# Performance work log

Hardware: AMD Instinct MI355X
Metric: run time of the kernel (lower is better)

Reference implementation:

```python
import jax, jax.numpy as jnp
import numpy as np

B, D, HID = 16384, 1024, 4096
HALF = D // 2


def setup_inputs() -> dict:
    key = jax.random.key(0)
    ks = jax.random.split(key, 9)
    sc_in = 1.0 / np.sqrt(HALF)
    sc_h = 1.0 / np.sqrt(HID)
    return {
        "z": jax.random.normal(ks[0], (B, D), dtype=jnp.float32),
        "W1s": jax.random.uniform(ks[1], (HALF, HID), jnp.float32, -sc_in, sc_in),
        "b1s": jax.random.uniform(ks[2], (HID,), jnp.float32, -sc_in, sc_in),
        "W2s": jax.random.uniform(ks[3], (HID, HALF), jnp.float32, -sc_h, sc_h),
        "b2s": jax.random.uniform(ks[4], (HALF,), jnp.float32, -sc_h, sc_h),
        "W1t": jax.random.uniform(ks[5], (HALF, HID), jnp.float32, -sc_in, sc_in),
        "b1t": jax.random.uniform(ks[6], (HID,), jnp.float32, -sc_in, sc_in),
        "W2t": jax.random.uniform(ks[7], (HID, HALF), jnp.float32, -sc_h, sc_h),
        "b2t": jax.random.uniform(ks[8], (HALF,), jnp.float32, -sc_h, sc_h),
    }


def reference(z, W1s, b1s, W2s, b2s, W1t, b1t, W2t, b2t):
    # mask_even=True: a = even-indexed features, b = odd-indexed features
    a = z[:, 0::2]  # [B, HALF]
    b = z[:, 1::2]  # [B, HALF]
    # two-layer MLPs for s and t (cond=None -> inp = a)
    s = jnp.maximum(a @ W1s + b1s, 0.0) @ W2s + b2s  # [B, HALF]
    t = jnp.maximum(a @ W1t + b1t, 0.0) @ W2t + b2t  # [B, HALF]
    b_out = b * jnp.exp(s) + t
    logdet = s.sum(axis=1)  # [B]
    # scatter back: a -> even slots, b_out -> odd slots (interleave)
    z_out = jnp.stack([a, b_out], axis=-1).reshape(z.shape)
    return z_out, logdet
```

## Files before the change

### kernel.cpp

```cpp
#include <hip/hip_runtime.h>
#include <hip/hip_bf16.h>
#include <cstdint>
#include <cstddef>

#define BROWS  16384
#define DDIM   1024
#define HID_N  4096
#define HALF_K 512
#define LDH    8192

typedef __attribute__((ext_vector_type(8))) short s8v;
typedef __attribute__((ext_vector_type(4))) float f4v;
typedef __attribute__((ext_vector_type(2))) float f2v;

__device__ __forceinline__ void gload16(const void* g, void* l) {
  __builtin_amdgcn_global_load_lds(
      (const __attribute__((address_space(1))) unsigned int*)g,
      (__attribute__((address_space(3))) unsigned int*)l, 16, 0, 0);
}
#define BAR()   asm volatile("s_barrier" ::: "memory")
#define BARS()  asm volatile("s_waitcnt lgkmcnt(0)\n\ts_barrier" ::: "memory")
#define SCHED0() __builtin_amdgcn_sched_barrier(0)

template <int N> __device__ __forceinline__ void vmw() {
  if constexpr (N == 0)      asm volatile("s_waitcnt vmcnt(0)" ::: "memory");
  else if constexpr (N == 4) asm volatile("s_waitcnt vmcnt(4)" ::: "memory");
  else if constexpr (N == 8) asm volatile("s_waitcnt vmcnt(8)" ::: "memory");
}

__device__ __forceinline__ void transpose_body(const float* __restrict__ W,
                                               __hip_bfloat16* __restrict__ WT,
                                               int K, int N, int bx, int by) {
  __shared__ float tile[32][33];
  const int n0 = bx * 32, k0 = by * 32;
  const int tx = threadIdx.x & 31;
  const int ty = threadIdx.x >> 5;
#pragma unroll
  for (int i = 0; i < 32; i += 8)
    tile[ty + i][tx] = W[(size_t)(k0 + ty + i) * N + n0 + tx];
  __syncthreads();
#pragma unroll
  for (int i = 0; i < 32; i += 8)
    WT[(size_t)(n0 + ty + i) * K + k0 + tx] = __float2bfloat16(tile[tx][ty + i]);
}

__global__ __launch_bounds__(256) void prep_kernel(const float* __restrict__ z,
                                                   __hip_bfloat16* __restrict__ a16,
                                                   const float* __restrict__ W1s,
                                                   const float* __restrict__ W1t,
                                                   const float* __restrict__ W2s,
                                                   const float* __restrict__ W2t,
                                                   __hip_bfloat16* __restrict__ w1T,
                                                   __hip_bfloat16* __restrict__ w2sT,
                                                   __hip_bfloat16* __restrict__ w2tT) {
  const int b = blockIdx.x;
  if (b < 4096) {
    const int idx = b * 256 + threadIdx.x;
    const int m  = idx >> 6;
    const int kb = idx & 63;
    const float4* zp = (const float4*)(z + (size_t)m * DDIM + (size_t)kb * 16);
    alignas(16) __hip_bfloat16 t[8];
#pragma unroll
    for (int i = 0; i < 4; ++i) {
      float4 v = zp[i];
      t[2 * i]     = __float2bfloat16(v.x);
      t[2 * i + 1] = __float2bfloat16(v.z);
    }
    *(s8v*)(a16 + (size_t)m * HALF_K + kb * 8) = *(const s8v*)t;
  } else if (b < 6144) {
    const int v = b - 4096;
    transpose_body(W1s, w1T, HALF_K, HID_N, v & 127, v >> 7);
  } else if (b < 8192) {
    const int v = b - 6144;
    transpose_body(W1t, w1T + (size_t)HID_N * HALF_K, HALF_K, HID_N, v & 127, v >> 7);
  } else if (b < 10240) {
    const int v = b - 8192;
    transpose_body(W2s, w2sT, HID_N, HALF_K, v & 15, v >> 4);
  } else {
    const int v = b - 10240;
    transpose_body(W2t, w2tT, HID_N, HALF_K, v & 15, v >> 4);
  }
}

__global__ __launch_bounds__(512, 2)
void gemm1_kernel(const __hip_bfloat16* __restrict__ A,
                  const __hip_bfloat16* __restrict__ BT,
                  const float* __restrict__ b1s, const float* __restrict__ b1t,
                  __hip_bfloat16* __restrict__ Hout) {
  __shared__ alignas(16) char smem[131072];
  constexpr int NT = HALF_K / 64;

  const int nwg = gridDim.x;
  const int orig = blockIdx.x;
  const int vid = (orig & 7) * (nwg >> 3) + (orig >> 3);
  const int bx = vid >> 5, by = vid & 31;
  const int m0 = bx * 256, n0 = by * 256;

  const int tid = threadIdx.x;
  const int trow = tid >> 3;
  const int scol = ((tid & 7) * 16) ^ ((trow & 7) << 4);

  const int lane = tid & 63, wid = tid >> 6;
  const int wr = wid >> 2, wc = wid & 3;
  const int lr = lane & 15, lk = lane >> 4;
  const int xo = (lr & 7) << 4;

  int aoff[4][2], boff[2][2];
#pragma unroll
  for (int j = 0; j < 4; ++j)
#pragma unroll
    for (int kk = 0; kk < 2; ++kk)
      aoff[j][kk] = (j * 32 + wr * 16 + lr) * 128 + ((kk * 64 + lk * 16) ^ xo);
#pragma unroll
  for (int nn = 0; nn < 2; ++nn)
#pragma unroll
    for (int kk = 0; kk < 2; ++kk)
      boff[nn][kk] = (nn * 64 + wc * 16 + lr) * 128 + ((kk * 64 + lk * 16) ^ xo);

  f4v acc[8][4] = {};

  auto stage_A = [&](int h, int T) {
#pragma unroll
    for (int l = 0; l < 2; ++l)
      gload16((const char*)A + (size_t)(m0 + h * 128 + l * 64 + trow) * (HALF_K * 2) + (size_t)T * 128 + scol,
              smem + (T & 1) * 65536 + h * 16384 + l * 8192 + tid * 16);
  };
  auto stage_B = [&](int h, int T) {
#pragma unroll
    for (int l = 0; l < 2; ++l)
      gload16((const char*)BT + (size_t)(n0 + h * 128 + l * 64 + trow) * (HALF_K * 2) + (size_t)T * 128 + scol,
              smem + (T & 1) * 65536 + 32768 + h * 16384 + l * 8192 + tid * 16);
  };

  stage_A(0, 0); stage_B(0, 0); stage_A(1, 0); stage_B(1, 0);
  stage_A(0, 1); stage_B(0, 1);
  vmw<4>();
  BAR();

  for (int T = 0; T < NT; ++T) {
    const char* bufp = smem + (T & 1) * 65536;
    s8v af[4][2], b0r[2][2], b1r[2][2];

#pragma unroll
    for (int j = 0; j < 4; ++j) {
      af[j][0] = *(const s8v*)(bufp + aoff[j][0]);
      af[j][1] = *(const s8v*)(bufp + aoff[j][1]);
    }
#pragma unroll
    for (int nn = 0; nn < 2; ++nn) {
      b0r[nn][0] = *(const s8v*)(bufp + 32768 + boff[nn][0]);
      b0r[nn][1] = *(const s8v*)(bufp + 32768 + boff[nn][1]);
    }
    if (T + 1 < NT) stage_B(1, T + 1);
    BAR(); SCHED0();
    __builtin_amdgcn_s_setprio(1);
#pragma unroll
    for (int j = 0; j < 4; ++j)
#pragma unroll
      for (int nn = 0; nn < 2; ++nn)
#pragma unroll
        for (int kk = 0; kk < 2; ++kk)
          acc[j][nn] = __builtin_amdgcn_mfma_f32_16x16x32_bf16(af[j][kk], b0r[nn][kk], acc[j][nn], 0, 0, 0);
    __builtin_amdgcn_s_setprio(0);
    BAR();

#pragma unroll
    for (int nn = 0; nn < 2; ++nn) {
      b1r[nn][0] = *(const s8v*)(bufp + 49152 + boff[nn][0]);
      b1r[nn][1] = *(const s8v*)(bufp + 49152 + boff[nn][1]);
    }
    if (T + 1 < NT) stage_A(1, T + 1);
    BAR(); SCHED0();
    __builtin_amdgcn_s_setprio(1);
#pragma unroll
    for (int j = 0; j < 4; ++j)
#pragma unroll
      for (int nn = 0; nn < 2; ++nn)
#pragma unroll
        for (int kk = 0; kk < 2; ++kk)
          acc[j][2 + nn] = __builtin_amdgcn_mfma_f32_16x16x32_bf16(af[j][kk], b1r[nn][kk], acc[j][2 + nn], 0, 0, 0);
    __builtin_amdgcn_s_setprio(0);
    BAR();

#pragma unroll
    for (int j = 0; j < 4; ++j) {
      af[j][0] = *(const s8v*)(bufp + 16384 + aoff[j][0]);
      af[j][1] = *(const s8v*)(bufp + 16384 + aoff[j][1]);
    }
    if (T + 2 < NT) stage_A(0, T + 2);
    BAR(); SCHED0();
    __builtin_amdgcn_s_setprio(1);
#pragma unroll
    for (int j = 0; j < 4; ++j)
#pragma unroll
      for (int nn = 0; nn < 2; ++nn)
#pragma unroll
        for (int kk = 0; kk < 2; ++kk)
          acc[4 + j][nn] = __builtin_amdgcn_mfma_f32_16x16x32_bf16(af[j][kk], b0r[nn][kk], acc[4 + j][nn], 0, 0, 0);
    __builtin_amdgcn_s_setprio(0);
    BAR();

    if (T + 2 < NT) stage_B(0, T + 2);
    SCHED0();
    __builtin_amdgcn_s_setprio(1);
#pragma unroll
    for (int j = 0; j < 4; ++j)
#pragma unroll
      for (int nn = 0; nn < 2; ++nn)
#pragma unroll
        for (int kk = 0; kk < 2; ++kk)
          acc[4 + j][2 + nn] = __builtin_amdgcn_mfma_f32_16x16x32_bf16(af[j][kk], b1r[nn][kk], acc[4 + j][2 + nn], 0, 0, 0);
    __builtin_amdgcn_s_setprio(0);
    if (T + 2 >= NT) vmw<0>(); else vmw<4>();
    BAR();
  }

  const float* bp = (n0 < HID_N) ? b1s : b1t;
  const int cb0 = n0 & (HID_N - 1);
  float bv[4];
#pragma unroll
  for (int ni = 0; ni < 4; ++ni) bv[ni] = bp[cb0 + ni * 64 + wc * 16 + lr];

#pragma unroll
  for (int mi = 0; mi < 8; ++mi) {
#pragma unroll
    for (int ni = 0; ni < 4; ++ni) {
      const int cb = (ni * 64 + wc * 16 + lr) * 2;
#pragma unroll
      for (int r = 0; r < 4; ++r) {
        const int row = mi * 32 + wr * 16 + lk * 4 + r;
        const int swz = ((row & 7) << 4) ^ (((row >> 3) & 1) << 8);
        float v = fmaxf(acc[mi][ni][r] + bv[ni], 0.0f);
        *(__hip_bfloat16*)(smem + row * 512 + (cb ^ swz)) = __float2bfloat16(v);
      }
    }
  }
  BARS();
#pragma unroll
  for (int i = 0; i < 16; ++i) {
    const int bo = tid * 16 + i * 8192;
    const int row = bo >> 9, cb = bo & 511;
    const int swz = ((row & 7) << 4) ^ (((row >> 3) & 1) << 8);
    s8v v = *(const s8v*)(smem + row * 512 + (cb ^ swz));
    *(s8v*)((char*)Hout + ((size_t)(m0 + row) * LDH + n0) * 2 + cb) = v;
  }
}

__global__ __launch_bounds__(512, 2)
void gemm2_kernel(const __hip_bfloat16* __restrict__ H,
                  const __hip_bfloat16* __restrict__ BsT,
                  const __hip_bfloat16* __restrict__ BtT,
                  const float* __restrict__ b2s, const float* __restrict__ b2t,
                  const float* __restrict__ zin, float* __restrict__ zout,
                  float* __restrict__ gpart) {
  __shared__ alignas(16) char smem[131072];
  constexpr int NT = HID_N / 64;

  const int nwg = gridDim.x;
  const int orig = blockIdx.x;
  const int vid = (orig & 7) * (nwg >> 3) + (orig >> 3);
  const int rb = vid >> 2, by = vid & 3;
  const int m0 = rb * 128, n0c = by * 128;

  const int tid = threadIdx.x;
  const int trow = tid >> 3;
  const int scol = ((tid & 7) * 16) ^ ((trow & 7) << 4);

  const int lane = tid & 63, wid = tid >> 6;
  const int ws = wid & 1, wc = (wid >> 1) & 1, wr = (wid >> 2) & 1;
  const int lr = lane & 15, lk = lane >> 4;
  const int xo = (lr & 7) << 4;

  const int aBase = ws ? 16384 : 0;
  const int bBase = ws ? 49152 : 32768;
  int aoff[4][2], boff[4][2];
#pragma unroll
  for (int f = 0; f < 4; ++f)
#pragma unroll
    for (int kk = 0; kk < 2; ++kk) {
      aoff[f][kk] = aBase + (wr * 64 + f * 16 + lr) * 128 + ((kk * 64 + lk * 16) ^ xo);
      boff[f][kk] = bBase + (wc * 64 + f * 16 + lr) * 128 + ((kk * 64 + lk * 16) ^ xo);
    }

  f4v acc[4][4] = {};

  auto stage_all = [&](int T) {
    char* dst = smem + (T & 1) * 65536;
    const size_t tcol = (size_t)T * 128 + scol;
#pragma unroll
    for (int l = 0; l < 2; ++l)
      gload16((const char*)H + (size_t)(m0 + l * 64 + trow) * (LDH * 2) + tcol,
              dst + l * 8192 + tid * 16);
#pragma unroll
    for (int l = 0; l < 2; ++l)
      gload16((const char*)H + (size_t)(m0 + l * 64 + trow) * (LDH * 2) + 8192 + tcol,
              dst + 16384 + l * 8192 + tid * 16);
#pragma unroll
    for (int l = 0; l < 2; ++l)
      gload16((const char*)BsT + (size_t)(n0c + l * 64 + trow) * (HID_N * 2) + tcol,
              dst + 32768 + l * 8192 + tid * 16);
#pragma unroll
    for (int l = 0; l < 2; ++l)
      gload16((const char*)BtT + (size_t)(n0c + l * 64 + trow) * (HID_N * 2) + tcol,
              dst + 49152 + l * 8192 + tid * 16);
  };

  stage_all(0);
  vmw<0>();
  BAR();

  for (int T = 0; T < NT; ++T) {
    const char* bufp = smem + (T & 1) * 65536;
    s8v af[4], bf[4];

#pragma unroll
    for (int f = 0; f < 4; ++f) af[f] = *(const s8v*)(bufp + aoff[f][0]);
#pragma unroll
    for (int f = 0; f < 4; ++f) bf[f] = *(const s8v*)(bufp + boff[f][0]);
    if (T + 1 < NT) stage_all(T + 1);
    __builtin_amdgcn_s_setprio(1);
#pragma unroll
    for (int fm = 0; fm < 4; ++fm)
#pragma unroll
      for (int fn = 0; fn < 4; ++fn)
        acc[fm][fn] = __builtin_amdgcn_mfma_f32_16x16x32_bf16(af[fm], bf[fn], acc[fm][fn], 0, 0, 0);
    __builtin_amdgcn_s_setprio(0);

#pragma unroll
    for (int f = 0; f < 4; ++f) af[f] = *(const s8v*)(bufp + aoff[f][1]);
#pragma unroll
    for (int f = 0; f < 4; ++f) bf[f] = *(const s8v*)(bufp + boff[f][1]);
    __builtin_amdgcn_s_setprio(1);
#pragma unroll
    for (int fm = 0; fm < 4; ++fm)
#pragma unroll
      for (int fn = 0; fn < 4; ++fn)
        acc[fm][fn] = __builtin_amdgcn_mfma_f32_16x16x32_bf16(af[fm], bf[fn], acc[fm][fn], 0, 0, 0);
    __builtin_amdgcn_s_setprio(0);

    if (T + 1 < NT) vmw<0>();
    BAR();
  }

  const float* bp2 = ws ? b2t : b2s;
  float bv[4];
#pragma unroll
  for (int fn = 0; fn < 4; ++fn) bv[fn] = bp2[n0c + wc * 64 + fn * 16 + lr];

  float* slds = (float*)smem;
  if (ws == 0) {
#pragma unroll
    for (int fm = 0; fm < 4; ++fm)
#pragma unroll
      for (int fn = 0; fn < 4; ++fn)
#pragma unroll
        for (int r = 0; r < 4; ++r) {
          const int row = wr * 64 + fm * 16 + lk * 4 + r;
          const int col = wc * 64 + fn * 16 + lr;
          slds[row * 128 + col] = acc[fm][fn][r] + bv[fn];
        }
  }
  BARS();
  if (ws == 1) {
    float pl[4][4] = {};
#pragma unroll
    for (int fm = 0; fm < 4; ++fm) {
#pragma unroll
      for (int fn = 0; fn < 4; ++fn) {
#pragma unroll
        for (int r = 0; r < 4; ++r) {
          const int row = wr * 64 + fm * 16 + lk * 4 + r;
          const int col = wc * 64 + fn * 16 + lr;
          const int rr = m0 + row;
          const float sv = slds[row * 128 + col];
          const float tv = acc[fm][fn][r] + bv[fn];
          pl[fm][r] += sv;
          const size_t base = (size_t)rr * DDIM + 2 * (size_t)(n0c + col);
          float2 zv = *(const float2*)(zin + base);
          f2v o;
          o.x = zv.x;
          o.y = zv.y * __expf(sv) + tv;
          __builtin_nontemporal_store(o, (f2v*)(zout + base));
        }
      }
    }
#pragma unroll
    for (int m = 1; m < 16; m <<= 1)
#pragma unroll
      for (int fm = 0; fm < 4; ++fm)
#pragma unroll
        for (int r = 0; r < 4; ++r)
          pl[fm][r] += __shfl_xor(pl[fm][r], m, 64);
    if (lr == 0) {
#pragma unroll
      for (int fm = 0; fm < 4; ++fm)
#pragma unroll
        for (int r = 0; r < 4; ++r) {
          const int rr = m0 + wr * 64 + fm * 16 + lk * 4 + r;
          gpart[(size_t)rr * 8 + by * 2 + wc] = pl[fm][r];
        }
    }
  }
}

__global__ __launch_bounds__(256) void ld_reduce_kernel(const float* __restrict__ gpart,
                                                        float* __restrict__ ld) {
  const int r = blockIdx.x * 256 + threadIdx.x;
  const float4* g = (const float4*)(gpart + (size_t)r * 8);
  float4 v0 = g[0], v1 = g[1];
  ld[r] = ((v0.x + v0.y) + (v0.z + v0.w)) + ((v1.x + v1.y) + (v1.z + v1.w));
}

extern "C" void kernel_launch(void* const* d_in, const int* in_sizes, int n_in,
                              void* d_out, int out_size, void* d_ws, size_t ws_size,
                              hipStream_t stream) {
  const float* z   = (const float*)d_in[0];
  const float* W1s = (const float*)d_in[1];
  const float* b1s = (const float*)d_in[2];
  const float* W2s = (const float*)d_in[3];
  const float* b2s = (const float*)d_in[4];
  const float* W1t = (const float*)d_in[5];
  const float* b1t = (const float*)d_in[6];
  const float* W2t = (const float*)d_in[7];
  const float* b2t = (const float*)d_in[8];
  float* zout = (float*)d_out;
  float* ld   = zout + (size_t)BROWS * DDIM;

  char* ws = (char*)d_ws;
  __hip_bfloat16* a16    = (__hip_bfloat16*)ws;
  __hip_bfloat16* w1catT = (__hip_bfloat16*)(ws + 16777216);
  __hip_bfloat16* w2sT   = (__hip_bfloat16*)(ws + 25165824);
  __hip_bfloat16* w2tT   = (__hip_bfloat16*)(ws + 29360128);
  float*          gpart  = (float*)(ws + 33554432);
  char*           hbase  = ws + 34078720;

  int CH = 2048;
  for (int c = 8192; c >= 2048; c >>= 1) {
    if (34078720ull + (size_t)c * 16384ull <= ws_size) { CH = c; break; }
  }
  __hip_bfloat16* H = (__hip_bfloat16*)hbase;

  prep_kernel<<<12288, 256, 0, stream>>>(z, a16, W1s, W1t, W2s, W2t,
                                         w1catT, w2sT, w2tT);

  const int SUB = (CH >= 4096) ? 4096 : CH;
  for (int mb = 0; mb < BROWS; mb += CH) {
    for (int sub = 0; sub < CH; sub += SUB) {
      gemm1_kernel<<<(SUB / 256) * 32, 512, 0, stream>>>(
          a16 + (size_t)(mb + sub) * HALF_K, w1catT, b1s, b1t,
          H + (size_t)sub * LDH);
    }
    gemm2_kernel<<<(CH / 128) * 4, 512, 0, stream>>>(
        H, w2sT, w2tT, b2s, b2t,
        z + (size_t)mb * DDIM, zout + (size_t)mb * DDIM, gpart + (size_t)mb * 8);
  }
  ld_reduce_kernel<<<BROWS / 256, 256, 0, stream>>>(gpart, ld);
}
```

Before: 358.6 us.

## Use 4-stage K=32 pipeline in gemm2 and pad epilogue LDS rows

Replaces gemm2's double-buffered K=64 tiles with a four-slot ring of K=32 tiles, prefetching three tiles ahead with partial vmcnt waits so global loads overlap more MFMA work. The LDS swizzle and fragment offsets are reworked for the 64-byte row stride. The epilogue's s-value staging buffer gets a 132-float row stride to avoid bank conflicts. The trade is twice as many barriers per K sweep and less MFMA work between each sync.

```diff
diff --git a/kernel.cpp b/kernel.cpp
--- a/kernel.cpp
+++ b/kernel.cpp
@@ -254,7 +254,7 @@
                   const float* __restrict__ zin, float* __restrict__ zout,
                   float* __restrict__ gpart) {
   __shared__ alignas(16) char smem[131072];
-  constexpr int NT = HID_N / 64;
+  constexpr int NT = HID_N / 32;
 
   const int nwg = gridDim.x;
   const int orig = blockIdx.x;
@@ -263,61 +263,46 @@
   const int m0 = rb * 128, n0c = by * 128;
 
   const int tid = threadIdx.x;
-  const int trow = tid >> 3;
-  const int scol = ((tid & 7) * 16) ^ ((trow & 7) << 4);
+  const int trow = tid >> 2;
+  const int scol = (((tid & 3) ^ ((tid >> 3) & 3)) << 4);
 
   const int lane = tid & 63, wid = tid >> 6;
   const int ws = wid & 1, wc = (wid >> 1) & 1, wr = (wid >> 2) & 1;
   const int lr = lane & 15, lk = lane >> 4;
-  const int xo = (lr & 7) << 4;
-
-  const int aBase = ws ? 16384 : 0;
-  const int bBase = ws ? 49152 : 32768;
-  int aoff[4][2], boff[4][2];
-#pragma unroll
-  for (int f = 0; f < 4; ++f)
-#pragma unroll
-    for (int kk = 0; kk < 2; ++kk) {
-      aoff[f][kk] = aBase + (wr * 64 + f * 16 + lr) * 128 + ((kk * 64 + lk * 16) ^ xo);
-      boff[f][kk] = bBase + (wc * 64 + f * 16 + lr) * 128 + ((kk * 64 + lk * 16) ^ xo);
-    }
+  const int xo2 = ((lr >> 1) & 3) << 4;
+
+  const int aBase = ws ? 8192 : 0;
+  const int bBase = ws ? 24576 : 16384;
+  int aoff[4], boff[4];
+#pragma unroll
+  for (int f = 0; f < 4; ++f) {
+    aoff[f] = aBase + (wr * 64 + f * 16 + lr) * 64 + ((lk * 16) ^ xo2);
+    boff[f] = bBase + (wc * 64 + f * 16 + lr) * 64 + ((lk * 16) ^ xo2);
+  }
 
   f4v acc[4][4] = {};
 
-  auto stage_all = [&](int T) {
-    char* dst = smem + (T & 1) * 65536;
-    const size_t tcol = (size_t)T * 128 + scol;
-#pragma unroll
-    for (int l = 0; l < 2; ++l)
-      gload16((const char*)H + (size_t)(m0 + l * 64 + trow) * (LDH * 2) + tcol,
-              dst + l * 8192 + tid * 16);
-#pragma unroll
-    for (int l = 0; l < 2; ++l)
-      gload16((const char*)H + (size_t)(m0 + l * 64 + trow) * (LDH * 2) + 8192 + tcol,
-              dst + 16384 + l * 8192 + tid * 16);
-#pragma unroll
-    for (int l = 0; l < 2; ++l)
-      gload16((const char*)BsT + (size_t)(n0c + l * 64 + trow) * (HID_N * 2) + tcol,
-              dst + 32768 + l * 8192 + tid * 16);
-#pragma unroll
-    for (int l = 0; l < 2; ++l)
-      gload16((const char*)BtT + (size_t)(n0c + l * 64 + trow) * (HID_N * 2) + tcol,
-              dst + 49152 + l * 8192 + tid * 16);
+  auto stage = [&](int T) {
+    char* dst = smem + (T & 3) * 32768;
+    const size_t tcol = (size_t)T * 64 + scol;
+    gload16((const char*)H + (size_t)(m0 + trow) * (LDH * 2) + tcol, dst + tid * 16);
+    gload16((const char*)H + (size_t)(m0 + trow) * (LDH * 2) + 8192 + tcol, dst + 8192 + tid * 16);
+    gload16((const char*)BsT + (size_t)(n0c + trow) * (HID_N * 2) + tcol, dst + 16384 + tid * 16);
+    gload16((const char*)BtT + (size_t)(n0c + trow) * (HID_N * 2) + tcol, dst + 24576 + tid * 16);
   };
 
-  stage_all(0);
-  vmw<0>();
+  stage(0); stage(1); stage(2);
+  vmw<8>();
   BAR();
 
   for (int T = 0; T < NT; ++T) {
-    const char* bufp = smem + (T & 1) * 65536;
+    const char* bufp = smem + (T & 3) * 32768;
     s8v af[4], bf[4];
-
-#pragma unroll
-    for (int f = 0; f < 4; ++f) af[f] = *(const s8v*)(bufp + aoff[f][0]);
-#pragma unroll
-    for (int f = 0; f < 4; ++f) bf[f] = *(const s8v*)(bufp + boff[f][0]);
-    if (T + 1 < NT) stage_all(T + 1);
+#pragma unroll
+    for (int f = 0; f < 4; ++f) af[f] = *(const s8v*)(bufp + aoff[f]);
+#pragma unroll
+    for (int f = 0; f < 4; ++f) bf[f] = *(const s8v*)(bufp + boff[f]);
+    if (T + 3 < NT) stage(T + 3);
     __builtin_amdgcn_s_setprio(1);
 #pragma unroll
     for (int fm = 0; fm < 4; ++fm)
@@ -325,20 +310,9 @@
       for (int fn = 0; fn < 4; ++fn)
         acc[fm][fn] = __builtin_amdgcn_mfma_f32_16x16x32_bf16(af[fm], bf[fn], acc[fm][fn], 0, 0, 0);
     __builtin_amdgcn_s_setprio(0);
-
-#pragma unroll
-    for (int f = 0; f < 4; ++f) af[f] = *(const s8v*)(bufp + aoff[f][1]);
-#pragma unroll
-    for (int f = 0; f < 4; ++f) bf[f] = *(const s8v*)(bufp + boff[f][1]);
-    __builtin_amdgcn_s_setprio(1);
-#pragma unroll
-    for (int fm = 0; fm < 4; ++fm)
-#pragma unroll
-      for (int fn = 0; fn < 4; ++fn)
-        acc[fm][fn] = __builtin_amdgcn_mfma_f32_16x16x32_bf16(af[fm], bf[fn], acc[fm][fn], 0, 0, 0);
-    __builtin_amdgcn_s_setprio(0);
-
-    if (T + 1 < NT) vmw<0>();
+    if (T + 3 < NT)      vmw<8>();
+    else if (T + 2 < NT) vmw<4>();
+    else if (T + 1 < NT) vmw<0>();
     BAR();
   }
 
@@ -357,7 +331,7 @@
         for (int r = 0; r < 4; ++r) {
           const int row = wr * 64 + fm * 16 + lk * 4 + r;
           const int col = wc * 64 + fn * 16 + lr;
-          slds[row * 128 + col] = acc[fm][fn][r] + bv[fn];
+          slds[row * 132 + col] = acc[fm][fn][r] + bv[fn];
         }
   }
   BARS();
@@ -372,7 +346,7 @@
           const int row = wr * 64 + fm * 16 + lk * 4 + r;
           const int col = wc * 64 + fn * 16 + lr;
           const int rr = m0 + row;
-          const float sv = slds[row * 128 + col];
+          const float sv = slds[row * 132 + col];
           const float tv = acc[fm][fn][r] + bv[fn];
           pl[fm][r] += sv;
           const size_t base = (size_t)rr * DDIM + 2 * (size_t)(n0c + col);
```

Measured after the change: 392.4 us. 1.09x slower.
